# Performance work log

Hardware: AMD Instinct MI355X
Metric: run time of the kernel (lower is better)

## Reference

```python
import jax, jax.numpy as jnp
import numpy as np

NUM_HEADS = 8


def _gaussian_mha(query, key, value, gaussian, key_padding_mask,
                  in_proj_weight, in_proj_bias, out_proj_weight, out_proj_bias):
    # query: [L, N, E]; key/value: [S, N, E]; gaussian: [N*H, L, S]; key_padding_mask: [N, S] bool
    L, N, E = query.shape
    S = key.shape[0]
    H = NUM_HEADS
    Dh = E // H
    scaling = float(Dh) ** -0.5

    # split the packed in-projection (torch layout: rows are [q; k; v], y = x @ W.T + b)
    wq, wk, wv = in_proj_weight[:E], in_proj_weight[E:2 * E], in_proj_weight[2 * E:]
    bq, bk, bv = in_proj_bias[:E], in_proj_bias[E:2 * E], in_proj_bias[2 * E:]

    q = (query @ wq.T + bq) * scaling          # [L, N, E]
    k = key @ wk.T + bk                        # [S, N, E]
    v = value @ wv.T + bv                      # [S, N, E]

    # -> [N*H, L, Dh] / [N*H, S, Dh] (matches torch view+transpose)
    q = jnp.transpose(q.reshape(L, N * H, Dh), (1, 0, 2))
    k = jnp.transpose(k.reshape(S, N * H, Dh), (1, 0, 2))
    v = jnp.transpose(v.reshape(S, N * H, Dh), (1, 0, 2))

    # scores with SMCA gaussian spatial bias added pre-softmax
    scores = jnp.einsum('bld,bsd->bls', q, k) + gaussian   # [N*H, L, S]

    # key padding mask: True -> -inf, broadcast over heads and queries
    mask = key_padding_mask[:, None, None, :]              # [N, 1, 1, S]
    scores = scores.reshape(N, H, L, S)
    scores = jnp.where(mask, -jnp.inf, scores).reshape(N * H, L, S)

    attn = jax.nn.softmax(scores, axis=-1)                 # [N*H, L, S]
    out = jnp.einsum('bls,bsd->bld', attn, v)              # [N*H, L, Dh]

    # back to [L, N, E] and output projection
    out = jnp.transpose(out, (1, 0, 2)).reshape(L, N, E)
    return out @ out_proj_weight.T + out_proj_bias


def setup_inputs() -> dict:
    key = jax.random.key(0)
    ks = jax.random.split(key, 8)
    L, S, N, E, H = 300, 1024, 32, 256, NUM_HEADS
    return {
        'query': jax.random.normal(ks[0], (L, N, E), jnp.float32),
        'key': jax.random.normal(ks[1], (S, N, E), jnp.float32),
        'value': jax.random.normal(ks[2], (S, N, E), jnp.float32),
        'gaussian': jax.random.normal(ks[3], (N * H, L, S), jnp.float32),
        'key_padding_mask': jnp.zeros((N, S), jnp.bool_),
        'in_proj_weight': jax.random.normal(ks[4], (3 * E, E), jnp.float32) * (E ** -0.5),
        'in_proj_bias': jax.random.normal(ks[5], (3 * E,), jnp.float32) * 0.02,
        'out_proj_weight': jax.random.normal(ks[6], (E, E), jnp.float32) * (E ** -0.5),
        'out_proj_bias': jax.random.normal(ks[7], (E,), jnp.float32) * 0.02,
    }


def reference(query, key, value, gaussian, key_padding_mask,
              in_proj_weight, in_proj_bias, out_proj_weight, out_proj_bias):
    return _gaussian_mha(query, key, value, gaussian, key_padding_mask,
                         in_proj_weight, in_proj_bias, out_proj_weight, out_proj_bias)
```

## Files before the change

kernel.cpp:

```cpp
#include <hip/hip_runtime.h>

#define LQ 300
#define NB 32
#define SK 1024
#define EE 256
#define HH 8
#define DH 32
#define BH 256
#define LPAD 304
#define NLT 19

typedef short short8 __attribute__((ext_vector_type(8)));
typedef short short4v __attribute__((ext_vector_type(4)));
typedef float f32x4 __attribute__((ext_vector_type(4)));

#define MFMA16(a, b, c) __builtin_amdgcn_mfma_f32_16x16x32_bf16((a), (b), (c), 0, 0, 0)

__device__ __forceinline__ short f2bf(float f) {
    unsigned u = __float_as_uint(f);
    u += 0x7FFFu + ((u >> 16) & 1u);
    return (short)(u >> 16);
}

__device__ __forceinline__ short8 cvt8(const float* __restrict__ p) {
    float4 x = *(const float4*)p;
    float4 y = *(const float4*)(p + 4);
    short8 r;
    r[0] = f2bf(x.x); r[1] = f2bf(x.y); r[2] = f2bf(x.z); r[3] = f2bf(x.w);
    r[4] = f2bf(y.x); r[5] = f2bf(y.y); r[6] = f2bf(y.z); r[7] = f2bf(y.w);
    return r;
}

__global__ __launch_bounds__(256) void prep_kernel(
    const float* __restrict__ ipw, const float* __restrict__ opw,
    short* __restrict__ wbf)
{
    int i = blockIdx.x * 256 + threadIdx.x;
    int base = i * 4;
    const float* src = (base < 3 * EE * EE) ? (ipw + base) : (opw + base - 3 * EE * EE);
    float4 x = *(const float4*)src;
    short4v r;
    r[0] = f2bf(x.x); r[1] = f2bf(x.y); r[2] = f2bf(x.z); r[3] = f2bf(x.w);
    *(short4v*)(wbf + base) = r;
}

__global__ __launch_bounds__(256) void proj_kernel(
    const float* __restrict__ query, const float* __restrict__ key,
    const float* __restrict__ value, const short* __restrict__ wbf,
    const float* __restrict__ bias,
    short* __restrict__ qws, short* __restrict__ kws, short* __restrict__ vws)
{
    int wave = (blockIdx.x * 256 + threadIdx.x) >> 6;
    int lid = threadIdx.x & 63, quad = lid >> 4, l16 = lid & 15;

    int u = wave, p;
    const float* X;
    if (u < 600)             { p = 0; X = query; }
    else if (u < 600 + 2048) { p = 1; X = key;   u -= 600; }
    else                     { p = 2; X = value; u -= 2648; }
    int t = u * 16 + l16;

    const short* wb = wbf + p * EE * EE;
    f32x4 acc[16];
    #pragma unroll
    for (int f = 0; f < 16; f++) acc[f] = (f32x4){0.f, 0.f, 0.f, 0.f};

    for (int ks = 0; ks < 8; ks++) {
        short8 af = cvt8(X + (size_t)t * EE + ks * 32 + quad * 8);
        #pragma unroll
        for (int f = 0; f < 16; f++) {
            short8 bf = *(const short8*)(wb + (size_t)(f * 16 + l16) * EE + ks * 32 + quad * 8);
            acc[f] = MFMA16(af, bf, acc[f]);
        }
    }

    int tokbase = (wave < 600 ? wave : u) * 16;
    #pragma unroll
    for (int f = 0; f < 16; f++) {
        int feat = f * 16 + l16;
        float bia = bias[p * EE + feat];
        int h = feat >> 5, d = feat & 31;
        #pragma unroll
        for (int r = 0; r < 4; r++) {
            int tok = tokbase + quad * 4 + r;
            float v = acc[f][r] + bia;
            int n = tok & 31, s = tok >> 5;
            int b = n * HH + h;
            if (p == 0) {
                v *= 0.17677669529663687f;
                qws[((size_t)b * LPAD + s) * DH + d] = f2bf(v);
            } else if (p == 1) {
                kws[((size_t)b * SK + s) * DH + d] = f2bf(v);
            } else {
                vws[((size_t)b * SK + s) * DH + d] = f2bf(v);
            }
        }
    }
}

__global__ __launch_bounds__(256) void vtrans_kernel(
    const short* __restrict__ vws, short* __restrict__ vt)
{
    __shared__ __align__(16) short tile[32][272];
    int b = blockIdx.x >> 2, s0 = (blockIdx.x & 3) * 256;
    const short* src = vws + ((size_t)b * SK + s0) * DH;
    #pragma unroll
    for (int pass = 0; pass < 4; pass++) {
        int i = pass * 256 + threadIdx.x;
        int sl = i >> 2, d0 = (i & 3) * 8;
        short8 x = *(const short8*)(src + sl * DH + d0);
        #pragma unroll
        for (int j = 0; j < 8; j++) tile[d0 + j][sl] = x[j];
    }
    __syncthreads();
    short* dst = vt + (size_t)b * DH * SK + s0;
    #pragma unroll
    for (int pass = 0; pass < 4; pass++) {
        int i = pass * 256 + threadIdx.x;
        int d = i >> 5, sl0 = (i & 31) * 8;
        *(short8*)(dst + (size_t)d * SK + sl0) = *(const short8*)(&tile[d][sl0]);
    }
}

__global__ __launch_bounds__(256) void attn_kernel(
    const short* __restrict__ qws, const short* __restrict__ kws,
    const short* __restrict__ vt, const float* __restrict__ gauss,
    const unsigned char* __restrict__ mask, short* __restrict__ ows)
{
    __shared__ __align__(16) short pbuf[4][16 * 80];
    __shared__ float obuf[4][16][32];
    __shared__ float mbuf[4][16];
    __shared__ float lbuf[4][16];

    int b = blockIdx.x / NLT, lt = blockIdx.x % NLT;
    int wv = threadIdx.x >> 6;
    int lid = threadIdx.x & 63, quad = lid >> 4, l16 = lid & 15;
    int n = b >> 3, h = b & 7;

    int ql = lt * 16 + l16;
    short8 qa = *(const short8*)(qws + ((size_t)b * LPAD + ql) * DH + quad * 8);

    f32x4 o0 = {0.f, 0.f, 0.f, 0.f}, o1 = {0.f, 0.f, 0.f, 0.f};
    float mr[4] = {-3e38f, -3e38f, -3e38f, -3e38f};
    float ls[4] = {0.f, 0.f, 0.f, 0.f};

    const float* gbase = gauss + (size_t)b * LQ * SK;
    const float* grow[4];
    #pragma unroll
    for (int r = 0; r < 4; r++) {
        int l = lt * 16 + quad * 4 + r;
        grow[r] = gbase + (size_t)(l < LQ ? l : LQ - 1) * SK + l16;
    }

    short* pb = pbuf[wv];
    int sw = quad << 4;
    int rw = (l16 >> 2) << 4;
    int sbase = wv * 256;

    for (int it = 0; it < 4; it++) {
        int sc = sbase + it * 64;

        short8 kb[4];
        #pragma unroll
        for (int c = 0; c < 4; c++)
            kb[c] = *(const short8*)(kws + ((size_t)b * SK + sc + c * 16 + l16) * DH + quad * 8);

        short8 vb[2][2];
        #pragma unroll
        for (int t2 = 0; t2 < 2; t2++)
            #pragma unroll
            for (int k2 = 0; k2 < 2; k2++)
                vb[t2][k2] = *(const short8*)(vt + ((size_t)b * DH + t2 * 16 + l16) * SK + sc + k2 * 32 + quad * 8);

        bool mk[4];
        #pragma unroll
        for (int c = 0; c < 4; c++) mk[c] = mask[n * SK + sc + c * 16 + l16] != 0;

        float g[4][4];
        #pragma unroll
        for (int r = 0; r < 4; r++)
            #pragma unroll
            for (int c = 0; c < 4; c++) g[r][c] = grow[r][sc + c * 16];

        f32x4 z = {0.f, 0.f, 0.f, 0.f};
        f32x4 cc[4];
        #pragma unroll
        for (int c = 0; c < 4; c++) cc[c] = MFMA16(qa, kb[c], z);

        float sv[4][4];
        #pragma unroll
        for (int r = 0; r < 4; r++)
            #pragma unroll
            for (int c = 0; c < 4; c++)
                sv[r][c] = mk[c] ? -3e38f : (cc[c][r] + g[r][c]);

        #pragma unroll
        for (int r = 0; r < 4; r++) {
            float mx = fmaxf(fmaxf(sv[r][0], sv[r][1]), fmaxf(sv[r][2], sv[r][3]));
            #pragma unroll
            for (int i = 1; i < 16; i <<= 1) mx = fmaxf(mx, __shfl_xor(mx, i, 64));
            float nm = fmaxf(mr[r], mx);
            float al = __expf(mr[r] - nm);
            float sm = 0.f;
            #pragma unroll
            for (int c = 0; c < 4; c++) { sv[r][c] = __expf(sv[r][c] - nm); sm += sv[r][c]; }
            #pragma unroll
            for (int i = 1; i < 16; i <<= 1) sm += __shfl_xor(sm, i, 64);
            ls[r] = ls[r] * al + sm;
            mr[r] = nm;
            o0[r] *= al; o1[r] *= al;
        }

        #pragma unroll
        for (int r = 0; r < 4; r++) {
            int row = quad * 4 + r;
            #pragma unroll
            for (int c = 0; c < 4; c++)
                pb[row * 80 + ((c * 16 + l16) ^ sw)] = f2bf(sv[r][c]);
        }
        short8 pa0 = *(const short8*)(pb + l16 * 80 + ((0 + quad * 8) ^ rw));
        short8 pa1 = *(const short8*)(pb + l16 * 80 + ((32 + quad * 8) ^ rw));

        o0 = MFMA16(pa0, vb[0][0], o0);
        o0 = MFMA16(pa1, vb[0][1], o0);
        o1 = MFMA16(pa0, vb[1][0], o1);
        o1 = MFMA16(pa1, vb[1][1], o1);
    }

    #pragma unroll
    for (int r = 0; r < 4; r++) {
        int row = quad * 4 + r;
        if (l16 == 0) { mbuf[wv][row] = mr[r]; lbuf[wv][row] = ls[r]; }
        obuf[wv][row][l16] = o0[r];
        obuf[wv][row][16 + l16] = o1[r];
    }
    __syncthreads();

    int row = threadIdx.x >> 4, col = threadIdx.x & 15;
    float M = -3e38f;
    #pragma unroll
    for (int w = 0; w < 4; w++) M = fmaxf(M, mbuf[w][row]);
    float L = 0.f, a0 = 0.f, a1 = 0.f;
    #pragma unroll
    for (int w = 0; w < 4; w++) {
        float e = __expf(mbuf[w][row] - M);
        L += e * lbuf[w][row];
        a0 += e * obuf[w][row][col];
        a1 += e * obuf[w][row][16 + col];
    }
    int l = lt * 16 + row;
    if (l < LQ) {
        float inv = 1.0f / L;
        size_t base = ((size_t)l * NB + n) * EE + h * DH;
        ows[base + col]      = f2bf(a0 * inv);
        ows[base + 16 + col] = f2bf(a1 * inv);
    }
}

__global__ __launch_bounds__(256) void oproj_kernel(
    const short* __restrict__ xa, const short* __restrict__ wbf,
    const float* __restrict__ bias, float* __restrict__ out)
{
    int wave = (blockIdx.x * 256 + threadIdx.x) >> 6;
    int lid = threadIdx.x & 63, quad = lid >> 4, l16 = lid & 15;
    int t = wave * 16 + l16;

    const short* wb = wbf + 3 * EE * EE;
    f32x4 acc[16];
    #pragma unroll
    for (int f = 0; f < 16; f++) acc[f] = (f32x4){0.f, 0.f, 0.f, 0.f};

    for (int ks = 0; ks < 8; ks++) {
        short8 af = *(const short8*)(xa + (size_t)t * EE + ks * 32 + quad * 8);
        #pragma unroll
        for (int f = 0; f < 16; f++) {
            short8 bf = *(const short8*)(wb + (size_t)(f * 16 + l16) * EE + ks * 32 + quad * 8);
            acc[f] = MFMA16(af, bf, acc[f]);
        }
    }

    #pragma unroll
    for (int f = 0; f < 16; f++) {
        int e = f * 16 + l16;
        float bi = bias[e];
        #pragma unroll
        for (int r = 0; r < 4; r++) {
            int tok = wave * 16 + quad * 4 + r;
            out[(size_t)tok * EE + e] = acc[f][r] + bi;
        }
    }
}

extern "C" void kernel_launch(void* const* d_in, const int* in_sizes, int n_in,
                              void* d_out, int out_size, void* d_ws, size_t ws_size,
                              hipStream_t stream) {
    const float* query = (const float*)d_in[0];
    const float* key   = (const float*)d_in[1];
    const float* value = (const float*)d_in[2];
    const float* gauss = (const float*)d_in[3];
    const unsigned char* mask = (const unsigned char*)d_in[4];
    const float* ipw = (const float*)d_in[5];
    const float* ipb = (const float*)d_in[6];
    const float* opw = (const float*)d_in[7];
    const float* opb = (const float*)d_in[8];
    float* out = (float*)d_out;

    short* wbf = (short*)d_ws;
    short* qws = wbf + 4 * EE * EE;
    short* kws = qws + (size_t)BH * LPAD * DH;
    short* vws = kws + (size_t)BH * SK * DH;
    short* vt  = vws + (size_t)BH * SK * DH;
    short* ows = vt  + (size_t)BH * SK * DH;

    prep_kernel<<<256, 256, 0, stream>>>(ipw, opw, wbf);
    proj_kernel<<<1174, 256, 0, stream>>>(query, key, value, wbf, ipb, qws, kws, vws);
    vtrans_kernel<<<1024, 256, 0, stream>>>(vws, vt);
    attn_kernel<<<BH * NLT, 256, 0, stream>>>(qws, kws, vt, gauss, mask, ows);
    oproj_kernel<<<150, 256, 0, stream>>>(ows, wbf, opb, out);
}
```

Before: 595.3 us.

## Transpose scores through LDS for row-per-lane softmax and swizzle block order

```diff
diff --git a/kernel.cpp b/kernel.cpp
--- a/kernel.cpp
+++ b/kernel.cpp
@@ -127,12 +127,14 @@
     const short* __restrict__ vt, const float* __restrict__ gauss,
     const unsigned char* __restrict__ mask, short* __restrict__ ows)
 {
-    __shared__ __align__(16) short pbuf[4][16 * 80];
-    __shared__ float obuf[4][16][32];
+    __shared__ __align__(16) float smem[4][16 * 64];
     __shared__ float mbuf[4][16];
     __shared__ float lbuf[4][16];
 
-    int b = blockIdx.x / NLT, lt = blockIdx.x % NLT;
+    int bid = blockIdx.x;
+    int swzb = (bid & 7) * ((BH * NLT) >> 3) + (bid >> 3);
+    int b = swzb / NLT, lt = swzb % NLT;
+
     int wv = threadIdx.x >> 6;
     int lid = threadIdx.x & 63, quad = lid >> 4, l16 = lid & 15;
     int n = b >> 3, h = b & 7;
@@ -141,8 +143,7 @@
     short8 qa = *(const short8*)(qws + ((size_t)b * LPAD + ql) * DH + quad * 8);
 
     f32x4 o0 = {0.f, 0.f, 0.f, 0.f}, o1 = {0.f, 0.f, 0.f, 0.f};
-    float mr[4] = {-3e38f, -3e38f, -3e38f, -3e38f};
-    float ls[4] = {0.f, 0.f, 0.f, 0.f};
+    float mr = -3e38f, ls = 0.f;
 
     const float* gbase = gauss + (size_t)b * LQ * SK;
     const float* grow[4];
@@ -152,10 +153,14 @@
         grow[r] = gbase + (size_t)(l < LQ ? l : LQ - 1) * SK + l16;
     }
 
-    short* pb = pbuf[wv];
-    int sw = quad << 4;
-    int rw = (l16 >> 2) << 4;
+    float* sl = smem[wv];
     int sbase = wv * 256;
+
+    int rk = l16 & 7;
+    int ra0 = l16 * 64 + (((quad * 2 + 0) ^ rk) << 2);
+    int ra1 = l16 * 64 + (((quad * 2 + 1) ^ rk) << 2);
+    int ra2 = l16 * 64 + (((quad * 2 + 8) ^ rk) << 2);
+    int ra3 = l16 * 64 + (((quad * 2 + 9) ^ rk) << 2);
 
     for (int it = 0; it < 4; it++) {
         int sc = sbase + it * 64;
@@ -187,39 +192,71 @@
         #pragma unroll
         for (int c = 0; c < 4; c++) cc[c] = MFMA16(qa, kb[c], z);
 
-        float sv[4][4];
-        #pragma unroll
-        for (int r = 0; r < 4; r++)
-            #pragma unroll
-            for (int c = 0; c < 4; c++)
-                sv[r][c] = mk[c] ? -3e38f : (cc[c][r] + g[r][c]);
-
-        #pragma unroll
-        for (int r = 0; r < 4; r++) {
-            float mx = fmaxf(fmaxf(sv[r][0], sv[r][1]), fmaxf(sv[r][2], sv[r][3]));
-            #pragma unroll
-            for (int i = 1; i < 16; i <<= 1) mx = fmaxf(mx, __shfl_xor(mx, i, 64));
-            float nm = fmaxf(mr[r], mx);
-            float al = __expf(mr[r] - nm);
-            float sm = 0.f;
-            #pragma unroll
-            for (int c = 0; c < 4; c++) { sv[r][c] = __expf(sv[r][c] - nm); sm += sv[r][c]; }
-            #pragma unroll
-            for (int i = 1; i < 16; i <<= 1) sm += __shfl_xor(sm, i, 64);
-            ls[r] = ls[r] * al + sm;
-            mr[r] = nm;
-            o0[r] *= al; o1[r] *= al;
-        }
-
         #pragma unroll
         for (int r = 0; r < 4; r++) {
             int row = quad * 4 + r;
+            int rowoff = row * 64;
+            int rkw = row & 7;
             #pragma unroll
-            for (int c = 0; c < 4; c++)
-                pb[row * 80 + ((c * 16 + l16) ^ sw)] = f2bf(sv[r][c]);
-        }
-        short8 pa0 = *(const short8*)(pb + l16 * 80 + ((0 + quad * 8) ^ rw));
-        short8 pa1 = *(const short8*)(pb + l16 * 80 + ((32 + quad * 8) ^ rw));
+            for (int c = 0; c < 4; c++) {
+                float s = mk[c] ? -3e38f : (cc[c][r] + g[r][c]);
+                int colg = c * 4 + (l16 >> 2);
+                sl[rowoff + (((colg ^ rkw) << 2) + (l16 & 3))] = s;
+            }
+        }
+
+        asm volatile("s_waitcnt lgkmcnt(0)" ::: "memory");
+
+        f32x4 s0 = *(const f32x4*)(sl + ra0);
+        f32x4 s1 = *(const f32x4*)(sl + ra1);
+        f32x4 s2 = *(const f32x4*)(sl + ra2);
+        f32x4 s3 = *(const f32x4*)(sl + ra3);
+
+        float mxa = fmaxf(fmaxf(fmaxf(s0[0], s0[1]), fmaxf(s0[2], s0[3])),
+                          fmaxf(fmaxf(s1[0], s1[1]), fmaxf(s1[2], s1[3])));
+        float mxb = fmaxf(fmaxf(fmaxf(s2[0], s2[1]), fmaxf(s2[2], s2[3])),
+                          fmaxf(fmaxf(s3[0], s3[1]), fmaxf(s3[2], s3[3])));
+        float mx = fmaxf(mxa, mxb);
+        mx = fmaxf(mx, __shfl_xor(mx, 16, 64));
+        mx = fmaxf(mx, __shfl_xor(mx, 32, 64));
+
+        float nm = fmaxf(mr, mx);
+        float al = __expf(mr - nm);
+
+        float p[16];
+        #pragma unroll
+        for (int j = 0; j < 4; j++) {
+            p[j]      = __expf(s0[j] - nm);
+            p[4 + j]  = __expf(s1[j] - nm);
+            p[8 + j]  = __expf(s2[j] - nm);
+            p[12 + j] = __expf(s3[j] - nm);
+        }
+        float sm = 0.f;
+        #pragma unroll
+        for (int j = 0; j < 16; j++) sm += p[j];
+        sm += __shfl_xor(sm, 16, 64);
+        sm += __shfl_xor(sm, 32, 64);
+
+        ls = ls * al + sm;
+        mr = nm;
+
+        int albits = __float_as_int(al);
+        #pragma unroll
+        for (int r = 0; r < 4; r++) {
+            float alr = __int_as_float(
+                __builtin_amdgcn_ds_bpermute(4 * (quad * 4 + r), albits));
+            o0[r] *= alr;
+            o1[r] *= alr;
+        }
+
+        short8 pa0, pa1;
+        #pragma unroll
+        for (int j = 0; j < 4; j++) {
+            pa0[j]     = f2bf(p[j]);
+            pa0[4 + j] = f2bf(p[4 + j]);
+            pa1[j]     = f2bf(p[8 + j]);
+            pa1[4 + j] = f2bf(p[12 + j]);
+        }
 
         o0 = MFMA16(pa0, vb[0][0], o0);
         o0 = MFMA16(pa1, vb[0][1], o0);
@@ -227,13 +264,14 @@
         o1 = MFMA16(pa1, vb[1][1], o1);
     }
 
+    asm volatile("s_waitcnt lgkmcnt(0)" ::: "memory");
     #pragma unroll
     for (int r = 0; r < 4; r++) {
         int row = quad * 4 + r;
-        if (l16 == 0) { mbuf[wv][row] = mr[r]; lbuf[wv][row] = ls[r]; }
-        obuf[wv][row][l16] = o0[r];
-        obuf[wv][row][16 + l16] = o1[r];
-    }
+        sl[row * 32 + l16]      = o0[r];
+        sl[row * 32 + 16 + l16] = o1[r];
+    }
+    if (quad == 0) { mbuf[wv][l16] = mr; lbuf[wv][l16] = ls; }
     __syncthreads();
 
     int row = threadIdx.x >> 4, col = threadIdx.x & 15;
@@ -245,8 +283,8 @@
     for (int w = 0; w < 4; w++) {
         float e = __expf(mbuf[w][row] - M);
         L += e * lbuf[w][row];
-        a0 += e * obuf[w][row][col];
-        a1 += e * obuf[w][row][16 + col];
+        a0 += e * smem[w][row * 32 + col];
+        a1 += e * smem[w][row * 32 + 16 + col];
     }
     int l = lt * 16 + row;
     if (l < LQ) {
```

New measurement: 592.0 us. No clear change (-0.6%).
